# Optimization experiments

Hardware: AMD Instinct MI355X
Metric: run time of the kernel (lower is better)

Reference implementation:

```python
import jax, jax.numpy as jnp
import numpy as np

N, E, B = 25000, 400000, 64          # nodes, edges, graphs
F, ED, H, C = 32, 8, 4, 32           # feature/edge dims, heads, per-head dim
HC = H * C
L = 4                                # init conv + 3 stacked convs (same shapes)
LIN = 128


def setup_inputs() -> dict:
    key = jax.random.key(0)
    ks = jax.random.split(key, 24)
    s = 0.05
    inp = {
        "x": jax.random.normal(ks[0], (N, F), jnp.float32),
        "edge_attr": jax.random.normal(ks[1], (E, ED), jnp.float32),
        "edge_index": jax.random.randint(ks[2], (2, E), 0, N),
        "batch_index": jnp.sort(jax.random.randint(ks[3], (N,), 0, B)),
        # stacked TransformerConv params (leading dim = layer)
        "Wq": jax.random.normal(ks[4], (L, F, HC), jnp.float32) * s,
        "bq": jnp.zeros((L, HC), jnp.float32),
        "Wk": jax.random.normal(ks[5], (L, F, HC), jnp.float32) * s,
        "bk": jnp.zeros((L, HC), jnp.float32),
        "Wv": jax.random.normal(ks[6], (L, F, HC), jnp.float32) * s,
        "bv": jnp.zeros((L, HC), jnp.float32),
        "We": jax.random.normal(ks[7], (L, ED, HC), jnp.float32) * s,
        "be": jnp.zeros((L, HC), jnp.float32),
        "Wskip": jax.random.normal(ks[8], (L, F, HC), jnp.float32) * s,
        "bskip": jnp.zeros((L, HC), jnp.float32),
        "Wbeta": jax.random.normal(ks[9], (L, 3 * HC, 1), jnp.float32) * s,
        # per-layer Linear(H*C -> emb) + BatchNorm
        "Wlin": jax.random.normal(ks[10], (L, HC, F), jnp.float32) * s,
        "blin": jnp.zeros((L, F), jnp.float32),
        "bn_gamma": jnp.ones((L, F), jnp.float32),
        "bn_beta": jnp.zeros((L, F), jnp.float32),
        # readout MLP
        "W1": jax.random.normal(ks[11], (2 * F, LIN), jnp.float32) * s,
        "b1": jnp.zeros((LIN,), jnp.float32),
        "W2": jax.random.normal(ks[12], (LIN, LIN // 2), jnp.float32) * s,
        "b2": jnp.zeros((LIN // 2,), jnp.float32),
        "W3": jax.random.normal(ks[13], (LIN // 2, 1), jnp.float32) * s,
        "b3": jnp.zeros((1,), jnp.float32),
    }
    return inp


def _transformer_conv(x, edge_attr, src, dst, Wq, bq, Wk, bk, Wv, bv, We, be,
                      Wskip, bskip, Wbeta):
    """PyG TransformerConv(heads=H, concat=True, beta=True, edge_dim=ED), eval mode."""
    n = x.shape[0]
    q = (x @ Wq + bq).reshape(n, H, C)
    k = (x @ Wk + bk).reshape(n, H, C)
    v = (x @ Wv + bv).reshape(n, H, C)
    e = (edge_attr @ We + be).reshape(-1, H, C)          # [E,H,C]
    kj = k[src] + e                                       # key_j + edge
    alpha = jnp.einsum('ehc,ehc->eh', q[dst], kj) / np.sqrt(C).astype(np.float32)
    # segment softmax over incoming edges per destination node
    amax = jax.ops.segment_max(alpha, dst, num_segments=n)
    a = jnp.exp(alpha - amax[dst])
    denom = jax.ops.segment_sum(a, dst, num_segments=n)
    a = a / denom[dst]                                    # [E,H]
    msg = (v[src] + e) * a[:, :, None]
    out = jax.ops.segment_sum(msg, dst, num_segments=n).reshape(n, HC)
    x_skip = x @ Wskip + bskip
    beta = jax.nn.sigmoid(
        jnp.concatenate([out, x_skip, out - x_skip], axis=-1) @ Wbeta)  # [N,1]
    return beta * x_skip + (1.0 - beta) * out


def _bn(h, gamma, beta):
    m = h.mean(axis=0)
    v = h.var(axis=0)
    return (h - m) * jax.lax.rsqrt(v + 1e-5) * gamma + beta


def reference(x, edge_attr, edge_index, batch_index,
              Wq, bq, Wk, bk, Wv, bv, We, be, Wskip, bskip, Wbeta,
              Wlin, blin, bn_gamma, bn_beta, W1, b1, W2, b2, W3, b3):
    src, dst = edge_index[0], edge_index[1]
    counts = jax.ops.segment_sum(jnp.ones((N,), jnp.float32), batch_index,
                                 num_segments=B)[:, None]
    h = x
    rep = jnp.zeros((B, 2 * F), jnp.float32)
    for i in range(L):
        h = _transformer_conv(h, edge_attr, src, dst,
                              Wq[i], bq[i], Wk[i], bk[i], Wv[i], bv[i],
                              We[i], be[i], Wskip[i], bskip[i], Wbeta[i])
        h = jax.nn.elu(h @ Wlin[i] + blin[i])
        h = _bn(h, bn_gamma[i], bn_beta[i])
        if i > 0:  # original pools only inside the n_layers loop
            gmx = jax.ops.segment_max(h, batch_index, num_segments=B)
            gmean = jax.ops.segment_sum(h, batch_index, num_segments=B) / counts
            rep = rep + jnp.concatenate([gmx, gmean], axis=1)
    z = jax.nn.elu(rep @ W1 + b1)
    z = jax.nn.elu(z @ W2 + b2)
    return z @ W3 + b3  # [B,1]
```

## Files before the change

kernel.cpp:

```cpp
#include <hip/hip_runtime.h>
#include <hip/hip_bf16.h>
#include <hip/hip_fp16.h>
#include <math.h>

#define NN 25000
#define EE 400000
#define BB 64
#define FF 32
#define EDD 8
#define HH 4
#define CC 32
#define HCC 128
#define LL 4
#define LINN 128

#define RSQRT_C 0.17677669529663687f
#define NREP 16
#define LSTATS_WORDS (NREP * 64)


__global__ void deg_kernel(const int* __restrict__ dst, int* __restrict__ deg) {
    int i = blockIdx.x * blockDim.x + threadIdx.x;
    if (i < EE) atomicAdd(&deg[dst[i]], 1);
}

__global__ void gstart_kernel(const int* __restrict__ bidx, int* __restrict__ gstart) {
    int b = threadIdx.x;
    if (b <= BB) {
        int lo = 0, hi = NN;
        while (lo < hi) { int mid = (lo + hi) >> 1; if (bidx[mid] < b) lo = mid + 1; else hi = mid; }
        gstart[b] = lo;
    }
}

__global__ void scan1_kernel(const int* __restrict__ deg, int* __restrict__ rowp, int* __restrict__ blks) {
    __shared__ int s[256];
    int i = blockIdx.x * 256 + threadIdx.x;
    int v = (i < NN) ? deg[i] : 0;
    s[threadIdx.x] = v;
    __syncthreads();
    for (int off = 1; off < 256; off <<= 1) {
        int t = (threadIdx.x >= off) ? s[threadIdx.x - off] : 0;
        __syncthreads();
        s[threadIdx.x] += t;
        __syncthreads();
    }
    if (i < NN) rowp[i + 1] = s[threadIdx.x];
    if (threadIdx.x == 255) blks[blockIdx.x] = s[255];
    if (i == 0) rowp[0] = 0;
}

__global__ void scan2_kernel(int* __restrict__ blks, int nb) {
    __shared__ int s[128];
    int t = threadIdx.x;
    int v = (t < nb) ? blks[t] : 0;
    s[t] = v;
    __syncthreads();
    for (int off = 1; off < 128; off <<= 1) {
        int u = (t >= off) ? s[t - off] : 0;
        __syncthreads();
        s[t] += u;
        __syncthreads();
    }
    if (t < nb) blks[t] = s[t] - v;
}

__global__ void scan3_kernel(int* __restrict__ rowp, const int* __restrict__ blks) {
    int i = blockIdx.x * 256 + threadIdx.x;
    if (i < NN) rowp[i + 1] += blks[blockIdx.x];
}

__global__ void fill_kernel(const int* __restrict__ dst, const int* __restrict__ rowp,
                            int* __restrict__ cnt2, int* __restrict__ eid) {
    int i = blockIdx.x * blockDim.x + threadIdx.x;
    if (i < EE) {
        int d = dst[i];
        int pos = rowp[d] + atomicAdd(&cnt2[d], 1);
        eid[pos] = i;
    }
}

__global__ void sortseg_kernel(const int* __restrict__ rowp, int* __restrict__ eid) {
    int n = blockIdx.x * 256 + threadIdx.x;
    if (n >= NN) return;
    int b = rowp[n], e = rowp[n + 1];
    int d = e - b;
    if (d <= 1) return;
    if (d <= 64) {
        int buf[64];
        for (int i = 0; i < d; ++i) buf[i] = eid[b + i];
        for (int i = 1; i < d; ++i) {
            int key = buf[i];
            int j = i - 1;
            while (j >= 0 && buf[j] > key) { buf[j + 1] = buf[j]; --j; }
            buf[j + 1] = key;
        }
        for (int i = 0; i < d; ++i) eid[b + i] = buf[i];
    } else {
        for (int i = b + 1; i < e; ++i) {
            int key = eid[i];
            int j = i - 1;
            while (j >= b && eid[j] > key) { eid[j + 1] = eid[j]; --j; }
            eid[j + 1] = key;
        }
    }
}

__global__ void csr_gather_kernel(const int* __restrict__ csre, const int* __restrict__ srcA,
                                  const float* __restrict__ eattr,
                                  int* __restrict__ csrsrc, uint4* __restrict__ eh) {
    int j = blockIdx.x * blockDim.x + threadIdx.x;
    if (j < EE) {
        int e = csre[j];
        csrsrc[j] = srcA[e];
        const float4* s = (const float4*)(eattr + (size_t)e * 8);
        float4 s0 = s[0], s1 = s[1];
        __half2 h0 = __float22half2_rn(make_float2(s0.x, s0.y));
        __half2 h1 = __float22half2_rn(make_float2(s0.z, s0.w));
        __half2 h2 = __float22half2_rn(make_float2(s1.x, s1.y));
        __half2 h3 = __float22half2_rn(make_float2(s1.z, s1.w));
        uint4 o;
        o.x = *(unsigned*)&h0; o.y = *(unsigned*)&h1;
        o.z = *(unsigned*)&h2; o.w = *(unsigned*)&h3;
        eh[j] = o;
    }
}

__global__ __launch_bounds__(256) void qkvs_kernel(
    const float* __restrict__ hin,
    const float* __restrict__ Wq, const float* __restrict__ bq,
    const float* __restrict__ Wk, const float* __restrict__ bk,
    const float* __restrict__ Wv, const float* __restrict__ bv,
    const float* __restrict__ Ws, const float* __restrict__ bs,
    __half2* __restrict__ qo, __half2* __restrict__ kvo,
    __half2* __restrict__ so, float* __restrict__ lstats)
{
    if (blockIdx.x == 0) {
        for (int i = threadIdx.x; i < LSTATS_WORDS; i += 256) lstats[i] = 0.0f;
    }
    __shared__ float xs[32][32];
    int lane = threadIdx.x & 63;
    int sel = threadIdx.x >> 6;
    const float* W = (sel == 0) ? Wq : (sel == 1) ? Wk : (sel == 2) ? Wv : Ws;
    const float* bias = (sel == 0) ? bq : (sel == 1) ? bk : (sel == 2) ? bv : bs;
    float w0[32], w1[32];
#pragma unroll
    for (int f = 0; f < 32; ++f) {
        float2 t = *(const float2*)&W[f * 128 + 2 * lane];
        w0[f] = t.x; w1[f] = t.y;
    }
    float2 bvv = *(const float2*)&bias[2 * lane];

    int c = lane >> 1;
    int pr = lane & 1;
    int h2k = c * 4 + pr;
    int h2v = c * 4 + 2 + pr;

    for (int chunk = blockIdx.x * 32; chunk < NN; chunk += gridDim.x * 32) {
        __syncthreads();
        for (int i = threadIdx.x; i < 1024; i += 256) {
            int nn = chunk + (i >> 5);
            xs[i >> 5][i & 31] = (nn < NN) ? hin[nn * 32 + (i & 31)] : 0.0f;
        }
        __syncthreads();
        int nmax = NN - chunk; if (nmax > 32) nmax = 32;
        for (int nl = 0; nl < nmax; ++nl) {
            float a0 = bvv.x, a1 = bvv.y;
#pragma unroll
            for (int f = 0; f < 32; ++f) {
                float xv = xs[nl][f];
                a0 += xv * w0[f];
                a1 += xv * w1[f];
            }
            size_t node = (size_t)(chunk + nl);
            __half2 hv = __float22half2_rn(make_float2(a0, a1));
            if (sel == 0)      qo[node * 64 + lane] = hv;
            else if (sel == 1) kvo[node * 128 + h2k] = hv;
            else if (sel == 2) kvo[node * 128 + h2v] = hv;
            else               so[node * 64 + lane] = hv;
        }
    }
}

__global__ __launch_bounds__(256) void attn_kernel(
    const uint2* __restrict__ qh, const uint4* __restrict__ kvb4,
    const uint2* __restrict__ skh,
    const uint4* __restrict__ eh,
    const int* __restrict__ srcArr,
    const int* __restrict__ rowp,
    const float* __restrict__ WeL, const float* __restrict__ beL,
    const float* __restrict__ WbL,
    const float* __restrict__ WlinL, const float* __restrict__ blinL,
    float* __restrict__ hlin, float* __restrict__ bnpart)
{
    __shared__ __align__(16) float shc[4 * 128];
    __shared__ float sbn[64];

    int tid = threadIdx.x;
    if (tid < 64) sbn[tid] = 0.0f;
    __syncthreads();

    int w = tid >> 6;
    int lane = tid & 63;
    int n = blockIdx.x * 4 + w;

    if (n < NN) {
        int c = lane & 31;
        int h = lane >> 5;

        float4 we[8];
#pragma unroll
        for (int d = 0; d < 8; ++d) we[d] = *(const float4*)&WeL[d * 128 + 4 * c];
        float4 be4 = *(const float4*)&beL[4 * c];

        uint2 qraw = qh[(size_t)n * 32 + c];
        float2 q01 = __half22float2(*(const __half2*)&qraw.x);
        float2 q23 = __half22float2(*(const __half2*)&qraw.y);
        float4 q4 = make_float4(q01.x * RSQRT_C, q01.y * RSQRT_C,
                                q23.x * RSQRT_C, q23.y * RSQRT_C);

        int beg = rowp[n], end = rowp[n + 1];
        int cnt = end - beg;
        int last = end - 1;

        float s = 0.0f, a0 = 0.0f, a1 = 0.0f, a2 = 0.0f, a3 = 0.0f;

        uint4 kvA = make_uint4(0u, 0u, 0u, 0u), kvB = kvA;
        uint4 eaA = kvA, eaB = kvA;
        int snC = 0, snD = 0;

        if (cnt > 0) {
            int j0 = beg + h;     j0 = (j0 < end) ? j0 : last;
            int j1 = beg + 2 + h; j1 = (j1 < end) ? j1 : last;
            int j2 = beg + 4 + h; j2 = (j2 < end) ? j2 : last;
            int j3 = beg + 6 + h; j3 = (j3 < end) ? j3 : last;
            int snA = srcArr[j0];
            int snB = srcArr[j1];
            snC = srcArr[j2];
            snD = srcArr[j3];
            kvA = kvb4[(size_t)snA * 32 + c];
            kvB = kvb4[(size_t)snB * 32 + c];
            eaA = eh[j0];
            eaB = eh[j1];
        }

        for (int jb = beg; jb < end; jb += 2) {
            int j = jb + h;
            uint4 kvC = kvb4[(size_t)snC * 32 + c];
            int jn = (j + 4 < end) ? j + 4 : last;
            uint4 eaC = eh[jn];
            int j8 = (j + 8 < end) ? j + 8 : last;
            int snE = srcArr[j8];

            float2 e01 = __half22float2(*(const __half2*)&eaA.x);
            float2 e23 = __half22float2(*(const __half2*)&eaA.y);
            float2 e45 = __half22float2(*(const __half2*)&eaA.z);
            float2 e67 = __half22float2(*(const __half2*)&eaA.w);
            float ead[8] = { e01.x, e01.y, e23.x, e23.y, e45.x, e45.y, e67.x, e67.y };

            float ex = be4.x, ey = be4.y, ez = be4.z, ew = be4.w;
#pragma unroll
            for (int d = 0; d < 8; ++d) {
                ex = fmaf(ead[d], we[d].x, ex);
                ey = fmaf(ead[d], we[d].y, ey);
                ez = fmaf(ead[d], we[d].z, ez);
                ew = fmaf(ead[d], we[d].w, ew);
            }

            float2 k01 = __half22float2(*(const __half2*)&kvA.x);
            float2 k23 = __half22float2(*(const __half2*)&kvA.y);
            float2 v01 = __half22float2(*(const __half2*)&kvA.z);
            float2 v23 = __half22float2(*(const __half2*)&kvA.w);

            float p = q4.x * (k01.x + ex) + q4.y * (k01.y + ey)
                    + q4.z * (k23.x + ez) + q4.w * (k23.y + ew);
            p += __shfl_xor(p, 1);
            p += __shfl_xor(p, 2);
            p += __shfl_xor(p, 4);
            float wg = (j < end) ? __expf(p) : 0.0f;
            s += wg;
            a0 = fmaf(wg, v01.x + ex, a0);
            a1 = fmaf(wg, v01.y + ey, a1);
            a2 = fmaf(wg, v23.x + ez, a2);
            a3 = fmaf(wg, v23.y + ew, a3);

            kvA = kvB; kvB = kvC;
            eaA = eaB; eaB = eaC;
            snC = snD; snD = snE;
        }

        s  += __shfl_xor(s, 32);
        a0 += __shfl_xor(a0, 32);
        a1 += __shfl_xor(a1, 32);
        a2 += __shfl_xor(a2, 32);
        a3 += __shfl_xor(a3, 32);

        float rs = (cnt > 0) ? (1.0f / s) : 0.0f;
        float o0 = a0 * rs, o1 = a1 * rs, o2 = a2 * rs, o3 = a3 * rs;

        uint2 skraw = skh[(size_t)n * 32 + c];
        float2 s01 = __half22float2(*(const __half2*)&skraw.x);
        float2 s23 = __half22float2(*(const __half2*)&skraw.y);
        float4 sk4 = make_float4(s01.x, s01.y, s23.x, s23.y);

        float4 wbo = *(const float4*)&WbL[4 * c];
        float4 wbs = *(const float4*)&WbL[128 + 4 * c];
        float4 wbd = *(const float4*)&WbL[256 + 4 * c];

        float t = o0 * wbo.x + sk4.x * wbs.x + (o0 - sk4.x) * wbd.x
                + o1 * wbo.y + sk4.y * wbs.y + (o1 - sk4.y) * wbd.y
                + o2 * wbo.z + sk4.z * wbs.z + (o2 - sk4.z) * wbd.z
                + o3 * wbo.w + sk4.w * wbs.w + (o3 - sk4.w) * wbd.w;
#pragma unroll
        for (int off = 1; off <= 16; off <<= 1) t += __shfl_xor(t, off);
        float beta = 1.0f / (1.0f + __expf(-t));
        float4 hc4;
        hc4.x = beta * sk4.x + (1.0f - beta) * o0;
        hc4.y = beta * sk4.y + (1.0f - beta) * o1;
        hc4.z = beta * sk4.z + (1.0f - beta) * o2;
        hc4.w = beta * sk4.w + (1.0f - beta) * o3;
        if (h == 0) ((float4*)shc)[w * 32 + c] = hc4;
        int cc = lane & 31;
        int half = lane >> 5;
        float acc = 0.0f;
#pragma unroll 8
        for (int i = 0; i < 64; ++i) {
            int ch = half * 64 + i;
            acc += shc[w * 128 + ch] * WlinL[ch * 32 + cc];
        }
        acc += __shfl_xor(acc, 32);
        if (lane < 32) {
            float hv = acc + blinL[lane];
            hv = (hv > 0.0f) ? hv : expm1f(hv);
            hlin[n * 32 + lane] = hv;
            atomicAdd(&sbn[lane], hv);
            atomicAdd(&sbn[32 + lane], hv * hv);
        }
    }
    __syncthreads();
    if (tid < 64) atomicAdd(&bnpart[(blockIdx.x & (NREP - 1)) * 64 + tid], sbn[tid]);
}

__global__ __launch_bounds__(256) void bnpool_kernel(
    const float* __restrict__ hlin, const float* __restrict__ bnpart,
    const float* __restrict__ gamma, const float* __restrict__ bnbeta,
    const int* __restrict__ gstart,
    float* __restrict__ hc, float* __restrict__ pool4, int doWrite)
{
    __shared__ float sscale[32], sshift[32];
    __shared__ float smax[8][32], ssum[8][32];
    int tid = threadIdx.x;
    int ch = tid & 31, row = tid >> 5;
    if (tid < 32) {
        float sm = 0.0f, sq = 0.0f;
#pragma unroll
        for (int r = 0; r < NREP; ++r) { sm += bnpart[r * 64 + tid]; sq += bnpart[r * 64 + 32 + tid]; }
        float mean = sm * (1.0f / NN);
        float var = sq * (1.0f / NN) - mean * mean;
        float scale = gamma[tid] * rsqrtf(var + 1e-5f);
        sscale[tid] = scale;
        sshift[tid] = bnbeta[tid] - mean * scale;
    }
    __syncthreads();
    int g = blockIdx.x >> 2;
    int chunk = blockIdx.x & 3;
    int gs = gstart[g], ge = gstart[g + 1];
    int len = ge - gs;
    int cs = gs + (len * chunk) / 4;
    int ce = gs + (len * (chunk + 1)) / 4;
    float scale = sscale[ch], shift = sshift[ch];
    float mx = -1e30f, sum = 0.0f;
    for (int n = cs + row; n < ce; n += 8) {
        float val = hlin[n * 32 + ch] * scale + shift;
        if (doWrite) hc[n * 32 + ch] = val;
        mx = fmaxf(mx, val);
        sum += val;
    }
    smax[row][ch] = mx; ssum[row][ch] = sum;
    __syncthreads();
    if (row == 0) {
#pragma unroll
        for (int r = 1; r < 8; ++r) { mx = fmaxf(mx, smax[r][ch]); sum += ssum[r][ch]; }
        pool4[(size_t)blockIdx.x * 64 + ch]      = mx;
        pool4[(size_t)blockIdx.x * 64 + 32 + ch] = sum;
    }
}

__global__ void pool_combine_kernel(const float* __restrict__ pool4,
                                    const int* __restrict__ gstart,
                                    float* __restrict__ rep) {
    int i = blockIdx.x * blockDim.x + threadIdx.x;
    if (i < BB * 32) {
        int g = i >> 5, ch = i & 31;
        int cntg = gstart[g + 1] - gstart[g];
        if (cntg > 0) {
            float mx = pool4[(size_t)(g * 4) * 64 + ch];
            float sum = pool4[(size_t)(g * 4) * 64 + 32 + ch];
#pragma unroll
            for (int k = 1; k < 4; ++k) {
                mx = fmaxf(mx, pool4[(size_t)(g * 4 + k) * 64 + ch]);
                sum += pool4[(size_t)(g * 4 + k) * 64 + 32 + ch];
            }
            rep[g * 64 + ch]      += mx;
            rep[g * 64 + 32 + ch] += sum / (float)cntg;
        }
    }
}

__device__ __forceinline__ float eluf(float x) { return x > 0.0f ? x : expm1f(x); }

__global__ __launch_bounds__(128) void readout_kernel(
    const float* __restrict__ rep,
    const float* __restrict__ W1, const float* __restrict__ b1,
    const float* __restrict__ W2, const float* __restrict__ b2,
    const float* __restrict__ W3, const float* __restrict__ b3,
    float* __restrict__ out)
{
    __shared__ float sr[64];
    __shared__ float sz1[128];
    __shared__ float sz2[64];
    int g = blockIdx.x;
    int t = threadIdx.x;
    if (t < 64) sr[t] = rep[g * 64 + t];
    __syncthreads();
    float acc = b1[t];
#pragma unroll 8
    for (int i = 0; i < 64; ++i) acc += sr[i] * W1[i * 128 + t];
    sz1[t] = eluf(acc);
    __syncthreads();
    if (t < 64) {
        float a2 = b2[t];
#pragma unroll 8
        for (int i = 0; i < 128; ++i) a2 += sz1[i] * W2[i * 64 + t];
        sz2[t] = eluf(a2);
    }
    __syncthreads();
    if (t < 64) {
        float p = sz2[t] * W3[t];
#pragma unroll
        for (int off = 1; off <= 32; off <<= 1) p += __shfl_xor(p, off);
        if (t == 0) out[g] = p + b3[0];
    }
}


extern "C" void kernel_launch(void* const* d_in, const int* in_sizes, int n_in,
                              void* d_out, int out_size, void* d_ws, size_t ws_size,
                              hipStream_t stream) {
    const float* x      = (const float*)d_in[0];
    const float* eattr  = (const float*)d_in[1];
    const int*   eidx   = (const int*)d_in[2];
    const int*   bidx   = (const int*)d_in[3];
    const float* Wq     = (const float*)d_in[4];
    const float* bq     = (const float*)d_in[5];
    const float* Wk     = (const float*)d_in[6];
    const float* bk     = (const float*)d_in[7];
    const float* Wv     = (const float*)d_in[8];
    const float* bv     = (const float*)d_in[9];
    const float* We     = (const float*)d_in[10];
    const float* be     = (const float*)d_in[11];
    const float* Wskip  = (const float*)d_in[12];
    const float* bskip  = (const float*)d_in[13];
    const float* Wbeta  = (const float*)d_in[14];
    const float* Wlin   = (const float*)d_in[15];
    const float* blin   = (const float*)d_in[16];
    const float* bng    = (const float*)d_in[17];
    const float* bnb    = (const float*)d_in[18];
    const float* W1     = (const float*)d_in[19];
    const float* b1     = (const float*)d_in[20];
    const float* W2     = (const float*)d_in[21];
    const float* b2     = (const float*)d_in[22];
    const float* W3     = (const float*)d_in[23];
    const float* b3     = (const float*)d_in[24];
    float* out = (float*)d_out;

    char* ws = (char*)d_ws;
    size_t off = 0;
    auto alloc = [&](size_t bytes) -> char* {
        char* p = ws + off;
        off = (off + bytes + 255) & ~(size_t)255;
        return p;
    };
    int*     rowp   = (int*)alloc((NN + 1) * 4);
    int*     degcnt = (int*)alloc(2 * NN * 4);
    int*     deg    = degcnt;
    int*     cnt2   = degcnt + NN;
    int*     csre   = (int*)alloc(EE * 4);
    int*     blks   = (int*)alloc(128 * 4);
    int*     gstart = (int*)alloc((BB + 1) * 4);
    float*   rep    = (float*)alloc(BB * 64 * 4);
    float*   pool4  = (float*)alloc(BB * 4 * 64 * 4);
    __half2* qH     = (__half2*)alloc((size_t)NN * 64 * 4);
    __half2* kvB    = (__half2*)alloc((size_t)NN * 128 * 4);
    __half2* skH    = (__half2*)alloc((size_t)NN * 64 * 4);
    float*   hlin   = (float*)alloc((size_t)NN * 32 * 4);
    float*   hcur   = (float*)alloc((size_t)NN * 32 * 4);
    float*   bnpart = (float*)alloc(LSTATS_WORDS * 4);
    int*     csrsrc = (int*)alloc(EE * 4);
    uint4*   ecsrh  = (uint4*)alloc((size_t)EE * 16);

    const int* srcA = eidx;
    const int* dstA = eidx + EE;

    (void)hipMemsetAsync(degcnt, 0, 2 * NN * 4, stream);
    (void)hipMemsetAsync(rep, 0, BB * 64 * 4, stream);

    deg_kernel<<<(EE + 255) / 256, 256, 0, stream>>>(dstA, deg);
    gstart_kernel<<<1, 128, 0, stream>>>(bidx, gstart);
    scan1_kernel<<<98, 256, 0, stream>>>(deg, rowp, blks);
    scan2_kernel<<<1, 128, 0, stream>>>(blks, 98);
    scan3_kernel<<<98, 256, 0, stream>>>(rowp, blks);
    fill_kernel<<<(EE + 255) / 256, 256, 0, stream>>>(dstA, rowp, cnt2, csre);
    sortseg_kernel<<<98, 256, 0, stream>>>(rowp, csre);
    csr_gather_kernel<<<(EE + 255) / 256, 256, 0, stream>>>(csre, srcA, eattr, csrsrc, ecsrh);

    const float* hin = x;
    for (int l = 0; l < LL; ++l) {
        qkvs_kernel<<<782, 256, 0, stream>>>(
            hin,
            Wq + l * FF * HCC, bq + l * HCC,
            Wk + l * FF * HCC, bk + l * HCC,
            Wv + l * FF * HCC, bv + l * HCC,
            Wskip + l * FF * HCC, bskip + l * HCC,
            qH, kvB, skH, bnpart);

        attn_kernel<<<(NN + 3) / 4, 256, 0, stream>>>(
            (const uint2*)qH, (const uint4*)kvB, (const uint2*)skH,
            ecsrh, csrsrc, rowp,
            We + l * EDD * HCC, be + l * HCC,
            Wbeta + l * 3 * HCC,
            Wlin + l * HCC * FF, blin + l * FF,
            hlin, bnpart);

        bnpool_kernel<<<BB * 4, 256, 0, stream>>>(hlin, bnpart, bng + l * FF, bnb + l * FF,
                                                  gstart, hcur, pool4, (l < LL - 1) ? 1 : 0);
        if (l > 0) {
            pool_combine_kernel<<<8, 256, 0, stream>>>(pool4, gstart, rep);
        }
        hin = hcur;
    }

    readout_kernel<<<64, 128, 0, stream>>>(rep, W1, b1, W2, b2, W3, b3, out);
}
```

Before: 545.3 us.

## Fold BatchNorm into next-layer load and pool via atomics in attention

Removes the separate BN-and-pool pass over node features. BN scale and shift are now computed by a tiny finalize kernel and applied on the fly when the next layer's QKV kernel loads its input. Graph max and sum pooling is done with replicated atomics (an order-preserving float-to-uint map for max) inside the attention epilogue, on pre-BN values, and the affine is applied afterwards. This cuts a full read and write of the node features per layer and some launches, and the gstart search is merged into the scan kernel. In exchange it adds global atomic contention and assumes a positive BN scale, since with a negative gamma the max of the affine would be wrong.

```diff
diff --git a/kernel.cpp b/kernel.cpp
--- a/kernel.cpp
+++ b/kernel.cpp
@@ -16,21 +16,15 @@
 
 #define RSQRT_C 0.17677669529663687f
 #define NREP 16
-#define LSTATS_WORDS (NREP * 64)
+#define NREPP 8
+#define GMAX_OFF (NREP * 64)
+#define GSUM_OFF (NREP * 64 + NREPP * BB * 32)
+#define LSTATS_WORDS (NREP * 64 + 2 * NREPP * BB * 32)
 
 
 __global__ void deg_kernel(const int* __restrict__ dst, int* __restrict__ deg) {
     int i = blockIdx.x * blockDim.x + threadIdx.x;
     if (i < EE) atomicAdd(&deg[dst[i]], 1);
-}
-
-__global__ void gstart_kernel(const int* __restrict__ bidx, int* __restrict__ gstart) {
-    int b = threadIdx.x;
-    if (b <= BB) {
-        int lo = 0, hi = NN;
-        while (lo < hi) { int mid = (lo + hi) >> 1; if (bidx[mid] < b) lo = mid + 1; else hi = mid; }
-        gstart[b] = lo;
-    }
 }
 
 __global__ void scan1_kernel(const int* __restrict__ deg, int* __restrict__ rowp, int* __restrict__ blks) {
@@ -50,7 +44,8 @@
     if (i == 0) rowp[0] = 0;
 }
 
-__global__ void scan2_kernel(int* __restrict__ blks, int nb) {
+__global__ void scan2_kernel(int* __restrict__ blks, int nb,
+                             const int* __restrict__ bidx, int* __restrict__ gstart) {
     __shared__ int s[128];
     int t = threadIdx.x;
     int v = (t < nb) ? blks[t] : 0;
@@ -63,6 +58,11 @@
         __syncthreads();
     }
     if (t < nb) blks[t] = s[t] - v;
+    if (t <= BB) {
+        int lo = 0, hi = NN;
+        while (lo < hi) { int mid = (lo + hi) >> 1; if (bidx[mid] < t) lo = mid + 1; else hi = mid; }
+        gstart[t] = lo;
+    }
 }
 
 __global__ void scan3_kernel(int* __restrict__ rowp, const int* __restrict__ blks) {
@@ -127,7 +127,7 @@
 }
 
 __global__ __launch_bounds__(256) void qkvs_kernel(
-    const float* __restrict__ hin,
+    const float* __restrict__ hin, int applyBN, const float* __restrict__ bnss,
     const float* __restrict__ Wq, const float* __restrict__ bq,
     const float* __restrict__ Wk, const float* __restrict__ bk,
     const float* __restrict__ Wv, const float* __restrict__ bv,
@@ -139,6 +139,8 @@
         for (int i = threadIdx.x; i < LSTATS_WORDS; i += 256) lstats[i] = 0.0f;
     }
     __shared__ float xs[32][32];
+    __shared__ float sbns[64];
+    if (threadIdx.x < 64) sbns[threadIdx.x] = applyBN ? bnss[threadIdx.x] : (threadIdx.x < 32 ? 1.0f : 0.0f);
     int lane = threadIdx.x & 63;
     int sel = threadIdx.x >> 6;
     const float* W = (sel == 0) ? Wq : (sel == 1) ? Wk : (sel == 2) ? Wv : Ws;
@@ -160,7 +162,9 @@
         __syncthreads();
         for (int i = threadIdx.x; i < 1024; i += 256) {
             int nn = chunk + (i >> 5);
-            xs[i >> 5][i & 31] = (nn < NN) ? hin[nn * 32 + (i & 31)] : 0.0f;
+            int ch = i & 31;
+            float v = (nn < NN) ? hin[nn * 32 + ch] : 0.0f;
+            xs[i >> 5][ch] = v * sbns[ch] + sbns[32 + ch];
         }
         __syncthreads();
         int nmax = NN - chunk; if (nmax > 32) nmax = 32;
@@ -182,16 +186,27 @@
     }
 }
 
+__device__ __forceinline__ unsigned fmap_u(float x) {
+    unsigned u = __float_as_uint(x);
+    return (u & 0x80000000u) ? ~u : (u | 0x80000000u);
+}
+__device__ __forceinline__ float funmap_u(unsigned u) {
+    unsigned b = (u & 0x80000000u) ? (u & 0x7fffffffu) : ~u;
+    return __uint_as_float(b);
+}
+
 __global__ __launch_bounds__(256) void attn_kernel(
     const uint2* __restrict__ qh, const uint4* __restrict__ kvb4,
     const uint2* __restrict__ skh,
     const uint4* __restrict__ eh,
     const int* __restrict__ srcArr,
     const int* __restrict__ rowp,
+    const int* __restrict__ bidx,
     const float* __restrict__ WeL, const float* __restrict__ beL,
     const float* __restrict__ WbL,
     const float* __restrict__ WlinL, const float* __restrict__ blinL,
-    float* __restrict__ hlin, float* __restrict__ bnpart)
+    float* __restrict__ hlin, float* __restrict__ lstats,
+    int doPool, int doWriteH)
 {
     __shared__ __align__(16) float shc[4 * 128];
     __shared__ float sbn[64];
@@ -332,77 +347,67 @@
         if (lane < 32) {
             float hv = acc + blinL[lane];
             hv = (hv > 0.0f) ? hv : expm1f(hv);
-            hlin[n * 32 + lane] = hv;
+            if (doWriteH) hlin[n * 32 + lane] = hv;
             atomicAdd(&sbn[lane], hv);
             atomicAdd(&sbn[32 + lane], hv * hv);
-        }
-    }
-    __syncthreads();
-    if (tid < 64) atomicAdd(&bnpart[(blockIdx.x & (NREP - 1)) * 64 + tid], sbn[tid]);
-}
-
-__global__ __launch_bounds__(256) void bnpool_kernel(
-    const float* __restrict__ hlin, const float* __restrict__ bnpart,
-    const float* __restrict__ gamma, const float* __restrict__ bnbeta,
-    const int* __restrict__ gstart,
-    float* __restrict__ hc, float* __restrict__ pool4, int doWrite)
-{
-    __shared__ float sscale[32], sshift[32];
-    __shared__ float smax[8][32], ssum[8][32];
-    int tid = threadIdx.x;
-    int ch = tid & 31, row = tid >> 5;
-    if (tid < 32) {
+            if (doPool) {
+                int g = bidx[n];
+                int repv = blockIdx.x & (NREPP - 1);
+                size_t idx = ((size_t)repv * BB + g) * 32 + lane;
+                atomicMax((unsigned*)lstats + GMAX_OFF + idx, fmap_u(hv));
+                atomicAdd(lstats + GSUM_OFF + idx, hv);
+            }
+        }
+    }
+    __syncthreads();
+    if (tid < 64) atomicAdd(&lstats[(blockIdx.x & (NREP - 1)) * 64 + tid], sbn[tid]);
+}
+
+__global__ void bnfin_kernel(const float* __restrict__ bnpart,
+                             const float* __restrict__ gamma, const float* __restrict__ bnbeta,
+                             float* __restrict__ bnss) {
+    int c = threadIdx.x;
+    if (c < 32) {
         float sm = 0.0f, sq = 0.0f;
 #pragma unroll
-        for (int r = 0; r < NREP; ++r) { sm += bnpart[r * 64 + tid]; sq += bnpart[r * 64 + 32 + tid]; }
+        for (int r = 0; r < NREP; ++r) { sm += bnpart[r * 64 + c]; sq += bnpart[r * 64 + 32 + c]; }
         float mean = sm * (1.0f / NN);
         float var = sq * (1.0f / NN) - mean * mean;
-        float scale = gamma[tid] * rsqrtf(var + 1e-5f);
-        sscale[tid] = scale;
-        sshift[tid] = bnbeta[tid] - mean * scale;
-    }
-    __syncthreads();
-    int g = blockIdx.x >> 2;
-    int chunk = blockIdx.x & 3;
-    int gs = gstart[g], ge = gstart[g + 1];
-    int len = ge - gs;
-    int cs = gs + (len * chunk) / 4;
-    int ce = gs + (len * (chunk + 1)) / 4;
-    float scale = sscale[ch], shift = sshift[ch];
-    float mx = -1e30f, sum = 0.0f;
-    for (int n = cs + row; n < ce; n += 8) {
-        float val = hlin[n * 32 + ch] * scale + shift;
-        if (doWrite) hc[n * 32 + ch] = val;
-        mx = fmaxf(mx, val);
-        sum += val;
-    }
-    smax[row][ch] = mx; ssum[row][ch] = sum;
-    __syncthreads();
-    if (row == 0) {
-#pragma unroll
-        for (int r = 1; r < 8; ++r) { mx = fmaxf(mx, smax[r][ch]); sum += ssum[r][ch]; }
-        pool4[(size_t)blockIdx.x * 64 + ch]      = mx;
-        pool4[(size_t)blockIdx.x * 64 + 32 + ch] = sum;
-    }
-}
-
-__global__ void pool_combine_kernel(const float* __restrict__ pool4,
-                                    const int* __restrict__ gstart,
-                                    float* __restrict__ rep) {
+        float scale = gamma[c] * rsqrtf(var + 1e-5f);
+        bnss[c] = scale;
+        bnss[32 + c] = bnbeta[c] - mean * scale;
+    }
+}
+
+__global__ void repupd_kernel(const float* __restrict__ lstats, const float* __restrict__ bnss,
+                              const int* __restrict__ gstart, float* __restrict__ rep, int assign) {
     int i = blockIdx.x * blockDim.x + threadIdx.x;
     if (i < BB * 32) {
         int g = i >> 5, ch = i & 31;
         int cntg = gstart[g + 1] - gstart[g];
+        float vmax = 0.0f, vmean = 0.0f;
         if (cntg > 0) {
-            float mx = pool4[(size_t)(g * 4) * 64 + ch];
-            float sum = pool4[(size_t)(g * 4) * 64 + 32 + ch];
-#pragma unroll
-            for (int k = 1; k < 4; ++k) {
-                mx = fmaxf(mx, pool4[(size_t)(g * 4 + k) * 64 + ch]);
-                sum += pool4[(size_t)(g * 4 + k) * 64 + 32 + ch];
+            const unsigned* gm = (const unsigned*)lstats + GMAX_OFF;
+            const float* gs = lstats + GSUM_OFF;
+            unsigned mx = 0u;
+            float sum = 0.0f;
+#pragma unroll
+            for (int r = 0; r < NREPP; ++r) {
+                size_t idx = ((size_t)r * BB + g) * 32 + ch;
+                unsigned m = gm[idx];
+                mx = (m > mx) ? m : mx;
+                sum += gs[idx];
             }
-            rep[g * 64 + ch]      += mx;
-            rep[g * 64 + 32 + ch] += sum / (float)cntg;
+            float scale = bnss[ch], shift = bnss[32 + ch];
+            vmax = scale * funmap_u(mx) + shift;
+            vmean = scale * (sum / (float)cntg) + shift;
+        }
+        if (assign) {
+            rep[g * 64 + ch] = vmax;
+            rep[g * 64 + 32 + ch] = vmean;
+        } else {
+            rep[g * 64 + ch] += vmax;
+            rep[g * 64 + 32 + ch] += vmean;
         }
     }
 }
@@ -489,13 +494,12 @@
     int*     blks   = (int*)alloc(128 * 4);
     int*     gstart = (int*)alloc((BB + 1) * 4);
     float*   rep    = (float*)alloc(BB * 64 * 4);
-    float*   pool4  = (float*)alloc(BB * 4 * 64 * 4);
     __half2* qH     = (__half2*)alloc((size_t)NN * 64 * 4);
     __half2* kvB    = (__half2*)alloc((size_t)NN * 128 * 4);
     __half2* skH    = (__half2*)alloc((size_t)NN * 64 * 4);
     float*   hlin   = (float*)alloc((size_t)NN * 32 * 4);
-    float*   hcur   = (float*)alloc((size_t)NN * 32 * 4);
-    float*   bnpart = (float*)alloc(LSTATS_WORDS * 4);
+    float*   lstats = (float*)alloc(LSTATS_WORDS * 4);
+    float*   bnss   = (float*)alloc(64 * 4);
     int*     csrsrc = (int*)alloc(EE * 4);
     uint4*   ecsrh  = (uint4*)alloc((size_t)EE * 16);
 
@@ -503,12 +507,10 @@
     const int* dstA = eidx + EE;
 
     (void)hipMemsetAsync(degcnt, 0, 2 * NN * 4, stream);
-    (void)hipMemsetAsync(rep, 0, BB * 64 * 4, stream);
 
     deg_kernel<<<(EE + 255) / 256, 256, 0, stream>>>(dstA, deg);
-    gstart_kernel<<<1, 128, 0, stream>>>(bidx, gstart);
     scan1_kernel<<<98, 256, 0, stream>>>(deg, rowp, blks);
-    scan2_kernel<<<1, 128, 0, stream>>>(blks, 98);
+    scan2_kernel<<<1, 128, 0, stream>>>(blks, 98, bidx, gstart);
     scan3_kernel<<<98, 256, 0, stream>>>(rowp, blks);
     fill_kernel<<<(EE + 255) / 256, 256, 0, stream>>>(dstA, rowp, cnt2, csre);
     sortseg_kernel<<<98, 256, 0, stream>>>(rowp, csre);
@@ -517,27 +519,28 @@
     const float* hin = x;
     for (int l = 0; l < LL; ++l) {
         qkvs_kernel<<<782, 256, 0, stream>>>(
-            hin,
+            (l == 0) ? x : hlin, (l > 0) ? 1 : 0, bnss,
             Wq + l * FF * HCC, bq + l * HCC,
             Wk + l * FF * HCC, bk + l * HCC,
             Wv + l * FF * HCC, bv + l * HCC,
             Wskip + l * FF * HCC, bskip + l * HCC,
-            qH, kvB, skH, bnpart);
+            qH, kvB, skH, lstats);
 
         attn_kernel<<<(NN + 3) / 4, 256, 0, stream>>>(
             (const uint2*)qH, (const uint4*)kvB, (const uint2*)skH,
-            ecsrh, csrsrc, rowp,
+            ecsrh, csrsrc, rowp, bidx,
             We + l * EDD * HCC, be + l * HCC,
             Wbeta + l * 3 * HCC,
             Wlin + l * HCC * FF, blin + l * FF,
-            hlin, bnpart);
-
-        bnpool_kernel<<<BB * 4, 256, 0, stream>>>(hlin, bnpart, bng + l * FF, bnb + l * FF,
-                                                  gstart, hcur, pool4, (l < LL - 1) ? 1 : 0);
+            hlin, lstats,
+            (l > 0) ? 1 : 0, (l < LL - 1) ? 1 : 0);
+
+        bnfin_kernel<<<1, 32, 0, stream>>>(lstats, bng + l * FF, bnb + l * FF, bnss);
+
         if (l > 0) {
-            pool_combine_kernel<<<8, 256, 0, stream>>>(pool4, gstart, rep);
-        }
-        hin = hcur;
+            repupd_kernel<<<8, 256, 0, stream>>>(lstats, bnss, gstart, rep, (l == 1) ? 1 : 0);
+        }
+        hin = hlin;
     }
 
     readout_kernel<<<64, 128, 0, stream>>>(rep, W1, b1, W2, b2, W3, b3, out);
```

Result: no change. 541.2 us (-0.7%).
